# Kernel tuning notes

Hardware: AMD Instinct MI355X
Metric: run time of the kernel (lower is better)

The kernel has to match this reference:

```python
import jax, jax.numpy as jnp
import numpy as np

B, T, H, W, D, NH = 8, 16, 14, 14, 768, 12
HID = int(D * 4.0)
HEAD_DIM = D // NH
EPS = 1e-5


def _ln(x, w, b):
    m = x.mean(-1, keepdims=True)
    v = ((x - m) ** 2).mean(-1, keepdims=True)
    return (x - m) * jax.lax.rsqrt(v + EPS) * w + b


def _attn(x, qkv_w, proj_w, proj_b):
    # x: [Bn, S, D]; qkv_w: [D, 3D] (no bias); proj: [D, D] + bias
    Bn, S, _ = x.shape
    qkv = (x @ qkv_w).reshape(Bn, S, 3, NH, HEAD_DIM).transpose(2, 0, 3, 1, 4)
    q, k, v = qkv[0], qkv[1], qkv[2]
    a = jnp.einsum('bhqd,bhkd->bhqk', q, k) * (HEAD_DIM ** -0.5)
    a = jax.nn.softmax(a, axis=-1)
    o = jnp.einsum('bhqk,bhkd->bhqd', a, v).transpose(0, 2, 1, 3).reshape(Bn, S, D)
    return o @ proj_w + proj_b


def setup_inputs() -> dict:
    key = jax.random.key(0)
    ks = jax.random.split(key, 20)
    N = H * W * T
    s = 0.02
    f32 = jnp.float32
    return {
        'x': jax.random.normal(ks[0], (B, 1 + N, D), f32),
        'tn1_w': jnp.ones((D,), f32), 'tn1_b': jnp.zeros((D,), f32),
        't_qkv_w': jax.random.normal(ks[1], (D, 3 * D), f32) * s,
        't_proj_w': jax.random.normal(ks[2], (D, D), f32) * s,
        't_proj_b': jnp.zeros((D,), f32),
        'tfc_w': jax.random.normal(ks[3], (D, D), f32) * s,
        'tfc_b': jnp.zeros((D,), f32),
        'n1_w': jnp.ones((D,), f32), 'n1_b': jnp.zeros((D,), f32),
        's_qkv_w': jax.random.normal(ks[4], (D, 3 * D), f32) * s,
        's_proj_w': jax.random.normal(ks[5], (D, D), f32) * s,
        's_proj_b': jnp.zeros((D,), f32),
        'n2_w': jnp.ones((D,), f32), 'n2_b': jnp.zeros((D,), f32),
        'fc1_w': jax.random.normal(ks[6], (D, HID), f32) * s,
        'fc1_b': jnp.zeros((HID,), f32),
        'fc2_w': jax.random.normal(ks[7], (HID, D), f32) * s,
        'fc2_b': jnp.zeros((D,), f32),
        'pt_mask': jnp.ones((B, 1 + N), dtype=bool),
        't_frames': T, 'height': H, 'width': W,
    }


def reference(x, tn1_w, tn1_b, t_qkv_w, t_proj_w, t_proj_b, tfc_w, tfc_b,
              n1_w, n1_b, s_qkv_w, s_proj_w, s_proj_b, n2_w, n2_b,
              fc1_w, fc1_b, fc2_w, fc2_b, pt_mask, t_frames, height, width):
    # divided space-time attention; USE_CLS_TOKEN=True, use_pt_visibility=False
    b = x.shape[0]
    t, h, w = t_frames, height, width
    n = h * w * t
    # --- temporal attention over t per (b, h, w) ---
    xt = x[:, 1:, :].reshape(b * h * w, t, D)  # 'b (h w t) m -> (b h w) t m'
    rt = _attn(_ln(xt, tn1_w, tn1_b), t_qkv_w, t_proj_w, t_proj_b)
    rt = rt.reshape(b, n, D) @ tfc_w + tfc_b  # temporal_fc
    xt2 = x[:, 1:, :] + rt
    init_cls = x[:, 0:1, :]  # [b, 1, D]
    # --- spatial attention over (1 + h*w) per (b, t) ---
    cls_tok = jnp.broadcast_to(init_cls, (b, t, D)).reshape(b * t, 1, D)
    xs = xt2.reshape(b, h * w, t, D).transpose(0, 2, 1, 3).reshape(b * t, h * w, D)
    xs = jnp.concatenate([cls_tok, xs], axis=1)  # [(b t), 1+hw, D]
    rs = _attn(_ln(xs, n1_w, n1_b), s_qkv_w, s_proj_w, s_proj_b)
    cls_out = rs[:, 0, :].reshape(b, t, D).mean(axis=1, keepdims=True)
    rs = rs[:, 1:, :].reshape(b, t, h * w, D).transpose(0, 2, 1, 3).reshape(b, n, D)
    x_new = jnp.concatenate([init_cls, xt2], axis=1) + jnp.concatenate([cls_out, rs], axis=1)
    # --- MLP block ---
    y = _ln(x_new, n2_w, n2_b)
    y = jax.nn.gelu(y @ fc1_w + fc1_b, approximate=False) @ fc2_w + fc2_b
    return x_new + y
```

## Files before the change

kernel.cpp:

```cpp
#include <hip/hip_runtime.h>
#include <cstdint>

using u16 = unsigned short;
using u32 = unsigned int;

typedef __bf16 bf16x8 __attribute__((ext_vector_type(8)));
typedef float  floatx4 __attribute__((ext_vector_type(4)));

#define DEV static __device__ __forceinline__

DEV u16 f2bf(float f) {
    u32 u = __float_as_uint(f);
    u += 0x7FFFu + ((u >> 16) & 1u);
    return (u16)(u >> 16);
}
DEV float bf2f(u16 v) { return __uint_as_float(((u32)v) << 16); }

DEV floatx4 mfma32(bf16x8 a, bf16x8 b, floatx4 c) {
    return __builtin_amdgcn_mfma_f32_16x16x32_bf16(a, b, c, 0, 0, 0);
}

DEV floatx4 fzero() { floatx4 z; z[0]=0.f; z[1]=0.f; z[2]=0.f; z[3]=0.f; return z; }

typedef __attribute__((address_space(3))) u32 as3_u32;
typedef __attribute__((address_space(1))) u32 as1_u32;

DEV void async_ld16(const u16* g, u16* l) {
    __builtin_amdgcn_global_load_lds(
        (const as1_u32*)g, (as3_u32*)l, 16, 0, 0);
}

__global__ __launch_bounds__(256) void transpose_w(
    const float* __restrict__ W, u16* __restrict__ Wt, int K, int N)
{
    __shared__ float t[32][33];
    const int tx = threadIdx.x, ty = threadIdx.y;
    const int gx = blockIdx.x * 32;
    const int gy = blockIdx.y * 32;
    #pragma unroll
    for (int i = 0; i < 4; ++i)
        t[ty + i*8][tx] = W[(size_t)(gy + ty + i*8) * N + gx + tx];
    __syncthreads();
    #pragma unroll
    for (int i = 0; i < 4; ++i)
        Wt[(size_t)(gx + ty + i*8) * K + gy + tx] = f2bf(t[tx][ty + i*8]);
}

template<int MODE>
__global__ __launch_bounds__(256) void ln_kernel(
    const float* __restrict__ xp, const u16* __restrict__ xt2,
    const float* __restrict__ w, const float* __restrict__ b,
    u16* __restrict__ out, int nrows)
{
    const int row = blockIdx.x * 4 + (threadIdx.x >> 6);
    if (row >= nrows) return;
    const int lane = threadIdx.x & 63;
    float vals[12];
    if constexpr (MODE == 0) {
        const float* src = xp + (size_t)(row + row/3136 + 1) * 768;
        #pragma unroll
        for (int j = 0; j < 3; ++j) {
            float4 v = reinterpret_cast<const float4*>(src)[j*64 + lane];
            vals[j*4+0]=v.x; vals[j*4+1]=v.y; vals[j*4+2]=v.z; vals[j*4+3]=v.w;
        }
    } else {
        const int bt = row / 197;
        const int p  = row - bt * 197;
        const int b0 = bt >> 4, tt = bt & 15;
        if (p == 0) {
            const float* src = xp + (size_t)b0 * 3137 * 768;
            #pragma unroll
            for (int j = 0; j < 3; ++j) {
                float4 v = reinterpret_cast<const float4*>(src)[j*64 + lane];
                vals[j*4+0]=v.x; vals[j*4+1]=v.y; vals[j*4+2]=v.z; vals[j*4+3]=v.w;
            }
        } else {
            const u16* src = xt2 + (size_t)(b0*3136 + (p-1)*16 + tt) * 768;
            #pragma unroll
            for (int j = 0; j < 3; ++j) {
                uint2 q = reinterpret_cast<const uint2*>(src)[j*64 + lane];
                vals[j*4+0] = bf2f((u16)(q.x & 0xFFFF));
                vals[j*4+1] = bf2f((u16)(q.x >> 16));
                vals[j*4+2] = bf2f((u16)(q.y & 0xFFFF));
                vals[j*4+3] = bf2f((u16)(q.y >> 16));
            }
        }
    }
    float s = 0.f, ss = 0.f;
    #pragma unroll
    for (int e = 0; e < 12; ++e) { s += vals[e]; ss += vals[e]*vals[e]; }
    #pragma unroll
    for (int o = 32; o > 0; o >>= 1) { s += __shfl_xor(s, o); ss += __shfl_xor(ss, o); }
    const float mean = s * (1.f/768.f);
    const float var  = ss * (1.f/768.f) - mean*mean;
    const float rstd = rsqrtf(var + 1e-5f);
    #pragma unroll
    for (int j = 0; j < 3; ++j) {
        const int c4 = (j*64 + lane) * 4;
        union { u16 u[4]; uint2 q; } o;
        #pragma unroll
        for (int e = 0; e < 4; ++e)
            o.u[e] = f2bf((vals[j*4+e] - mean)*rstd*w[c4+e] + b[c4+e]);
        *reinterpret_cast<uint2*>(&out[(size_t)row*768 + c4]) = o.q;
    }
}

__global__ __launch_bounds__(256) void combine_ln2(
    const float* __restrict__ xp, const u16* __restrict__ xt2,
    const u16* __restrict__ rsb, const float* __restrict__ w, const float* __restrict__ b,
    float* __restrict__ xnew, u16* __restrict__ ln2, int nrows)
{
    const int row = blockIdx.x * 4 + (threadIdx.x >> 6);
    if (row >= nrows) return;
    const int lane = threadIdx.x & 63;
    const int b0 = row / 3137;
    const int j  = row - b0 * 3137;
    float vals[12];
    if (j == 0) {
        #pragma unroll
        for (int e = 0; e < 12; ++e) {
            const int c = e*64 + lane;
            float acc = 0.f;
            for (int t = 0; t < 16; ++t)
                acc += bf2f(rsb[(size_t)(b0*16 + t) * 197 * 768 + c]);
            vals[e] = xp[(size_t)row*768 + c] + acc * (1.f/16.f);
        }
    } else {
        const int n_idx = j - 1;
        const int hw = n_idx >> 4, tt = n_idx & 15;
        const u16* a  = xt2 + (size_t)(b0*3136 + n_idx) * 768;
        const u16* r2 = rsb + (size_t)((b0*16 + tt)*197 + 1 + hw) * 768;
        #pragma unroll
        for (int e = 0; e < 12; ++e) {
            const int c = e*64 + lane;
            vals[e] = bf2f(a[c]) + bf2f(r2[c]);
        }
    }
    float s = 0.f, ss = 0.f;
    #pragma unroll
    for (int e = 0; e < 12; ++e) { s += vals[e]; ss += vals[e]*vals[e]; }
    #pragma unroll
    for (int o = 32; o > 0; o >>= 1) { s += __shfl_xor(s, o); ss += __shfl_xor(ss, o); }
    const float mean = s * (1.f/768.f);
    const float var  = ss * (1.f/768.f) - mean*mean;
    const float rstd = rsqrtf(var + 1e-5f);
    #pragma unroll
    for (int e = 0; e < 12; ++e) {
        const int c = e*64 + lane;
        xnew[(size_t)row*768 + c] = vals[e];
        ln2[(size_t)row*768 + c]  = f2bf((vals[e] - mean)*rstd*w[c] + b[c]);
    }
}


#define BARX() do { __builtin_amdgcn_sched_barrier(0); asm volatile("" ::: "memory"); \
    __builtin_amdgcn_s_barrier(); asm volatile("" ::: "memory"); \
    __builtin_amdgcn_sched_barrier(0); } while(0)
#define WAITL() do { asm volatile("s_waitcnt lgkmcnt(0)" ::: "memory"); \
    __builtin_amdgcn_sched_barrier(0); } while(0)
#define WAITV4() do { asm volatile("s_waitcnt vmcnt(4)" ::: "memory"); \
    __builtin_amdgcn_sched_barrier(0); } while(0)
#define WAITV0() do { asm volatile("s_waitcnt vmcnt(0)" ::: "memory"); \
    __builtin_amdgcn_sched_barrier(0); } while(0)

#define RD_A(d, mh) do { \
    _Pragma("unroll") for (int ff = 0; ff < 4; ++ff) { \
      _Pragma("unroll") for (int ks = 0; ks < 2; ++ks) { \
        const int rr = ((mh)*4 + ff)*16 + m15; \
        a[ff*2+ks] = *reinterpret_cast<const bf16x8*>( \
            &sm[(d)*32768 + wm*8192 + rr*64 + ((ks*4 + quad) ^ (m15 & 7))*8]); \
    } } } while(0)

#define RD_B(d, np) do { \
    _Pragma("unroll") for (int nn = 0; nn < 2; ++nn) { \
      _Pragma("unroll") for (int ks = 0; ks < 2; ++ks) { \
        const int rr = (wn & 1)*64 + ((np)*2 + nn)*16 + m15; \
        b[((np)*2 + nn)*2 + ks] = *reinterpret_cast<const bf16x8*>( \
            &sm[(d)*32768 + 16384 + (wn >> 1)*8192 + rr*64 + ((ks*4 + quad) ^ (m15 & 7))*8]); \
    } } } while(0)

#define MQ(F0, NF0) do { \
    _Pragma("unroll") for (int ff = 0; ff < 4; ++ff) { \
      _Pragma("unroll") for (int nn = 0; nn < 2; ++nn) { \
        floatx4 c_ = acc[(F0)+ff][(NF0)+nn]; \
        c_ = mfma32(a[ff*2+0], b[((NF0)+nn)*2+0], c_); \
        c_ = mfma32(a[ff*2+1], b[((NF0)+nn)*2+1], c_); \
        acc[(F0)+ff][(NF0)+nn] = c_; \
    } } } while(0)

#define PRIO1() __builtin_amdgcn_s_setprio(1)
#define PRIO0() __builtin_amdgcn_s_setprio(0)

#define ITER(tt, FULL) do { \
    const int d_ = (tt) & 1; \
     RD_A(d_, 0); RD_B(d_, 0); STAGE((tt)+1, 2); \
    BARX(); WAITL(); PRIO1(); MQ(0,0); PRIO0(); BARX(); \
     RD_B(d_, 1); STAGE((tt)+1, 3); \
    BARX(); WAITL(); PRIO1(); MQ(0,2); PRIO0(); BARX(); \
     RD_A(d_, 1); if (FULL) STAGE((tt)+2, 0); \
    BARX(); WAITL(); PRIO1(); MQ(4,2); PRIO0(); BARX(); \
     if (FULL) STAGE((tt)+2, 1); \
    BARX(); PRIO1(); MQ(4,0); PRIO0(); \
    if (FULL) WAITV4(); else WAITV0(); \
    BARX(); \
     RD_A(d_^1, 0); RD_B(d_^1, 0); if (FULL) STAGE((tt)+2, 2); \
    BARX(); WAITL(); PRIO1(); MQ(0,0); PRIO0(); BARX(); \
     RD_B(d_^1, 1); if (FULL) STAGE((tt)+2, 3); \
    BARX(); WAITL(); PRIO1(); MQ(0,2); PRIO0(); BARX(); \
     RD_A(d_^1, 1); if (FULL) STAGE((tt)+3, 0); \
    BARX(); WAITL(); PRIO1(); MQ(4,2); PRIO0(); BARX(); \
     if (FULL) STAGE((tt)+3, 1); \
    BARX(); PRIO1(); MQ(4,0); PRIO0(); \
    if (FULL) WAITV4(); \
    BARX(); \
} while(0)

template<int RESID, bool BIAS, bool GELU_ACT, bool OUTF, bool OUTB, bool MASKM>
__global__ __launch_bounds__(512, 2) void gemm256(
    const u16* __restrict__ A, const u16* __restrict__ Bt,
    const float* __restrict__ bias, const float* __restrict__ resid,
    float* __restrict__ Cf, u16* __restrict__ Cb,
    int N, int K, int lda, int ldb, int Mvalid)
{
    extern __shared__ u16 sm[];
    const int tid  = threadIdx.x;
    const int w    = tid >> 6;
    const int l    = tid & 63;
    const int m15  = l & 15;
    const int quad = l >> 4;
    const int wm   = w >> 2;
    const int wn   = w & 3;
    const long m0  = (long)blockIdx.y * 256;
    const long n0  = (long)blockIdx.x * 256;

    const int srow   = w*8 + (l >> 3);
    const int schunk = ((l & 7) ^ (l >> 3)) * 8;
    const u16* gA = A  + (size_t)(m0 + srow) * lda + schunk;
    const u16* gB = Bt + (size_t)(n0 + srow) * ldb + schunk;
    const int w512 = w * 512;

    auto STAGE = [&](int tt, int h4) {
        const int dd = tt & 1;
        const int k0 = tt << 6;
        const int h  = h4 & 1;
        if (h4 & 2) {
            const u16* g = gA + (size_t)(h * 128) * lda + k0;
            u16* lp = sm + dd*32768 + h*8192 + w512;
            async_ld16(g, lp);
            async_ld16(g + (size_t)(64 * lda), lp + 4096);
        } else {
            const u16* g = gB + (size_t)(h * 128) * ldb + k0;
            u16* lp = sm + dd*32768 + 16384 + h*8192 + w512;
            async_ld16(g, lp);
            async_ld16(g + (size_t)(64 * ldb), lp + 4096);
        }
    };

    bf16x8 a[8], b[8];
    floatx4 acc[8][4];
    #pragma unroll
    for (int f = 0; f < 8; ++f)
        #pragma unroll
        for (int nf = 0; nf < 4; ++nf) acc[f][nf] = fzero();

    const int NIT = K >> 7;

    STAGE(0, 0); STAGE(0, 1); STAGE(0, 2); STAGE(0, 3);
    STAGE(1, 0); STAGE(1, 1);
    WAITV4(); BARX();

    int t = 0;
    for (int i = 0; i < NIT - 1; ++i, t += 2) { ITER(t, 1); }
    ITER(t, 0);

    float bv[4];
    #pragma unroll
    for (int nf = 0; nf < 4; ++nf)
        bv[nf] = BIAS ? bias[n0 + wn*64 + nf*16 + m15] : 0.f;

    if constexpr (OUTB) {
        u16* cst = sm + w * 8192;
        #pragma unroll
        for (int f = 0; f < 8; ++f) {
            #pragma unroll
            for (int nf = 0; nf < 4; ++nf) {
                #pragma unroll
                for (int r = 0; r < 4; ++r) {
                    const long row = m0 + wm*128 + f*16 + quad*4 + r;
                    float v = acc[f][nf][r] + bv[nf];
                    if constexpr (RESID == 1)
                        v += resid[(size_t)row * N + (n0 + wn*64 + nf*16 + m15)];
                    if constexpr (RESID == 2)
                        v += resid[(size_t)(row + row/3136 + 1) * 768 + (n0 + wn*64 + nf*16 + m15)];
                    if constexpr (GELU_ACT)
                        v = 0.5f * v * (1.f + erff(v * 0.70710678118f));
                    cst[(f*16 + quad*4 + r)*64 + nf*16 + m15] = f2bf(v);
                }
            }
        }
        #pragma unroll
        for (int it = 0; it < 16; ++it) {
            const int lr = it*8 + (l >> 3);
            const long grow = m0 + wm*128 + lr;
            if constexpr (MASKM) { if (grow >= Mvalid) continue; }
            const int cc = (l & 7) * 8;
            *reinterpret_cast<uint4*>(&Cb[(size_t)grow * N + n0 + wn*64 + cc]) =
                *reinterpret_cast<const uint4*>(&cst[lr*64 + cc]);
        }
    } else {
        #pragma unroll
        for (int f = 0; f < 8; ++f) {
            #pragma unroll
            for (int nf = 0; nf < 4; ++nf) {
                const long col = n0 + wn*64 + nf*16 + m15;
                #pragma unroll
                for (int r = 0; r < 4; ++r) {
                    const long row = m0 + wm*128 + f*16 + quad*4 + r;
                    if constexpr (MASKM) { if (row >= Mvalid) continue; }
                    float v = acc[f][nf][r] + bv[nf];
                    if constexpr (RESID == 1) v += resid[(size_t)row * N + col];
                    if constexpr (RESID == 2) v += resid[(size_t)(row + row/3136 + 1) * 768 + col];
                    if constexpr (GELU_ACT)   v = 0.5f * v * (1.f + erff(v * 0.70710678118f));
                    if constexpr (OUTF) Cf[(size_t)row * N + col] = v;
                }
            }
        }
    }
}

template<int S, int NQ, int NIT>
__global__ __launch_bounds__(256) void attn_kernel(
    const u16* __restrict__ qkv, u16* __restrict__ out, int ntask)
{
    __shared__ __attribute__((aligned(16))) u16 P_lds[4][16*32];
    const int wave = threadIdx.x >> 6;
    const int lane = threadIdx.x & 63;
    const int task = blockIdx.x * 4 + wave;
    if (task >= ntask) return;
    const int seq  = task / (12 * NQ);
    const int rem  = task - seq * (12 * NQ);
    const int head = rem / NQ;
    const int qt   = rem - head * NQ;
    const int m15  = lane & 15;
    const int quad = lane >> 4;
    const size_t base = (size_t)seq * S;

    const u16* qp = qkv + (base + qt*16 + m15) * 2304 + head*64 + quad*8;
    const bf16x8 Qf0 = *reinterpret_cast<const bf16x8*>(qp);
    const bf16x8 Qf1 = *reinterpret_cast<const bf16x8*>(qp + 32);

    floatx4 Oacc[4];
    #pragma unroll
    for (int c = 0; c < 4; ++c) Oacc[c] = fzero();
    float mrun = -__builtin_inff();
    float lrun = 0.f;
    u16* P = &P_lds[wave][0];

    for (int it = 0; it < NIT; ++it) {
        const int j0 = it * 32;
        floatx4 st[2];
        #pragma unroll
        for (int h2 = 0; h2 < 2; ++h2) {
            const u16* kp = qkv + (base + j0 + h2*16 + m15) * 2304 + 768 + head*64 + quad*8;
            const bf16x8 K0 = *reinterpret_cast<const bf16x8*>(kp);
            const bf16x8 K1 = *reinterpret_cast<const bf16x8*>(kp + 32);
            floatx4 z = fzero();
            z = mfma32(K0, Qf0, z);
            st[h2] = mfma32(K1, Qf1, z);
        }
        float sc[8];
        #pragma unroll
        for (int h2 = 0; h2 < 2; ++h2)
            #pragma unroll
            for (int r = 0; r < 4; ++r) {
                const int jj = j0 + h2*16 + quad*4 + r;
                sc[h2*4+r] = (jj < S) ? st[h2][r] * 0.125f : -__builtin_inff();
            }
        float tmax = sc[0];
        #pragma unroll
        for (int k = 1; k < 8; ++k) tmax = fmaxf(tmax, sc[k]);
        tmax = fmaxf(tmax, __shfl_xor(tmax, 16));
        tmax = fmaxf(tmax, __shfl_xor(tmax, 32));
        const float mnew = fmaxf(mrun, tmax);
        float p[8], tsum = 0.f;
        #pragma unroll
        for (int k = 0; k < 8; ++k) { p[k] = __expf(sc[k] - mnew); tsum += p[k]; }
        tsum += __shfl_xor(tsum, 16);
        tsum += __shfl_xor(tsum, 32);
        const float alpha = __expf(mrun - mnew);
        lrun = lrun * alpha + tsum;
        mrun = mnew;
        #pragma unroll
        for (int r = 0; r < 4; ++r) {
            const float ar = __shfl(alpha, quad*4 + r);
            #pragma unroll
            for (int c = 0; c < 4; ++c) Oacc[c][r] *= ar;
        }
        #pragma unroll
        for (int h2 = 0; h2 < 2; ++h2)
            #pragma unroll
            for (int r = 0; r < 4; ++r)
                P[m15*32 + h2*16 + quad*4 + r] = f2bf(p[h2*4+r]);
        const bf16x8 Pf = *reinterpret_cast<const bf16x8*>(&P[m15*32 + quad*8]);
        #pragma unroll
        for (int c = 0; c < 4; ++c) {
            union { u16 u[8]; bf16x8 v; } vf;
            #pragma unroll
            for (int jj2 = 0; jj2 < 8; ++jj2)
                vf.u[jj2] = qkv[(base + j0 + quad*8 + jj2) * 2304 + 1536 + head*64 + c*16 + m15];
            Oacc[c] = mfma32(Pf, vf.v, Oacc[c]);
        }
    }
    const float linv_self = 1.f / lrun;
    #pragma unroll
    for (int r = 0; r < 4; ++r) {
        const int prow = qt*16 + quad*4 + r;
        const float linv = __shfl(linv_self, quad*4 + r);
        if (prow < S) {
            u16* op = out + (base + prow) * 768 + head*64 + m15;
            #pragma unroll
            for (int c = 0; c < 4; ++c) op[c*16] = f2bf(Oacc[c][r] * linv);
        }
    }
}

extern "C" void kernel_launch(void* const* d_in, const int* in_sizes, int n_in,
                              void* d_out, int out_size, void* d_ws, size_t ws_size,
                              hipStream_t stream)
{
    (void)in_sizes; (void)n_in; (void)out_size; (void)ws_size;
    const float* x        = (const float*)d_in[0];
    const float* tn1_w    = (const float*)d_in[1];
    const float* tn1_b    = (const float*)d_in[2];
    const float* t_qkv_w  = (const float*)d_in[3];
    const float* t_proj_w = (const float*)d_in[4];
    const float* t_proj_b = (const float*)d_in[5];
    const float* tfc_w    = (const float*)d_in[6];
    const float* tfc_b    = (const float*)d_in[7];
    const float* n1_w     = (const float*)d_in[8];
    const float* n1_b     = (const float*)d_in[9];
    const float* s_qkv_w  = (const float*)d_in[10];
    const float* s_proj_w = (const float*)d_in[11];
    const float* s_proj_b = (const float*)d_in[12];
    const float* n2_w     = (const float*)d_in[13];
    const float* n2_b     = (const float*)d_in[14];
    const float* fc1_w    = (const float*)d_in[15];
    const float* fc1_b    = (const float*)d_in[16];
    const float* fc2_w    = (const float*)d_in[17];
    const float* fc2_b    = (const float*)d_in[18];
    float* out = (float*)d_out;

    char* ws = (char*)d_ws;
    size_t off = 0;
    auto alloc = [&](size_t bytes) -> void* {
        void* p = ws + off;
        off += (bytes + 255) & ~(size_t)255;
        return p;
    };
    u16* wt_tqkv  = (u16*)alloc((size_t)768*2304*2);
    u16* wt_tproj = (u16*)alloc((size_t)768*768*2);
    u16* wt_tfc   = (u16*)alloc((size_t)768*768*2);
    u16* wt_sqkv  = (u16*)alloc((size_t)768*2304*2);
    u16* wt_sproj = (u16*)alloc((size_t)768*768*2);
    u16* wt_fc1   = (u16*)alloc((size_t)768*3072*2);
    u16* wt_fc2   = (u16*)alloc((size_t)3072*768*2);
    u16* slotA = (u16*)alloc((size_t)25280*2304*2);
    u16* slotB = (u16*)alloc((size_t)25216*768*2);
    u16* slotD = (u16*)alloc((size_t)25344*768*2);
    u16* slotE = (u16*)alloc((size_t)25216*768*2);

    dim3 tb(32, 8);
    transpose_w<<<dim3(72, 24), tb, 0, stream>>>(t_qkv_w,  wt_tqkv,  768, 2304);
    transpose_w<<<dim3(24, 24), tb, 0, stream>>>(t_proj_w, wt_tproj, 768, 768);
    transpose_w<<<dim3(24, 24), tb, 0, stream>>>(tfc_w,    wt_tfc,   768, 768);
    transpose_w<<<dim3(72, 24), tb, 0, stream>>>(s_qkv_w,  wt_sqkv,  768, 2304);
    transpose_w<<<dim3(24, 24), tb, 0, stream>>>(s_proj_w, wt_sproj, 768, 768);
    transpose_w<<<dim3(96, 24), tb, 0, stream>>>(fc1_w,    wt_fc1,   768, 3072);
    transpose_w<<<dim3(24, 96), tb, 0, stream>>>(fc2_w,    wt_fc2,   3072, 768);

    const size_t GLDS = 131072;

    u16* lnT  = slotD;
    u16* qkvT = slotA;
    ln_kernel<0><<<25088/4, 256, 0, stream>>>(x, nullptr, tn1_w, tn1_b, lnT, 25088);
    gemm256<0,false,false,false,true,false><<<dim3(9,98), 512, GLDS, stream>>>(
        lnT, wt_tqkv, nullptr, nullptr, nullptr, qkvT, 2304, 768, 768, 768, 0);

    u16* attnT = slotD;
    attn_kernel<16,1,1><<<18816/4, 256, 0, stream>>>(qkvT, attnT, 18816);

    u16* hp = slotE;
    gemm256<0,true,false,false,true,false><<<dim3(3,98), 512, GLDS, stream>>>(
        attnT, wt_tproj, t_proj_b, nullptr, nullptr, hp, 768, 768, 768, 768, 0);

    u16* xt2 = slotB;
    gemm256<2,true,false,false,true,false><<<dim3(3,98), 512, GLDS, stream>>>(
        hp, wt_tfc, tfc_b, x, nullptr, xt2, 768, 768, 768, 768, 0);

    u16* lnS = slotD;
    ln_kernel<1><<<25216/4, 256, 0, stream>>>(x, xt2, n1_w, n1_b, lnS, 25216);

    u16* qkvS = slotA;
    gemm256<0,false,false,false,true,true><<<dim3(9,99), 512, GLDS, stream>>>(
        lnS, wt_sqkv, nullptr, nullptr, nullptr, qkvS, 2304, 768, 768, 768, 25216);

    u16* attnS = slotD;
    attn_kernel<197,13,7><<<19968/4, 256, 0, stream>>>(qkvS, attnS, 19968);

    u16* rsb = slotE;
    gemm256<0,true,false,false,true,true><<<dim3(3,99), 512, GLDS, stream>>>(
        attnS, wt_sproj, s_proj_b, nullptr, nullptr, rsb, 768, 768, 768, 768, 25216);

    float* xnew = out;
    u16* ln2 = slotD;
    combine_ln2<<<25096/4, 256, 0, stream>>>(x, xt2, rsb, n2_w, n2_b, xnew, ln2, 25096);

    u16* h1 = slotA;
    for (int half = 0; half < 2; ++half) {
        const u16* w1h = wt_fc1 + (size_t)half * 1536 * 768;
        const float* b1h = fc1_b + half * 1536;
        gemm256<0,true,true,false,true,true><<<dim3(6,99), 512, GLDS, stream>>>(
            ln2, w1h, b1h, nullptr, nullptr, h1, 1536, 768, 768, 768, 25096);
        const u16* w2h = wt_fc2 + (size_t)half * 1536;
        if (half == 0)
            gemm256<1,true,false,true,false,true><<<dim3(3,99), 512, GLDS, stream>>>(
                h1, w2h, fc2_b, out, out, nullptr, 768, 1536, 1536, 3072, 25096);
        else
            gemm256<1,false,false,true,false,true><<<dim3(3,99), 512, GLDS, stream>>>(
                h1, w2h, nullptr, out, out, nullptr, 768, 1536, 1536, 3072, 25096);
    }
}
```

Measured before the change: 1.297 ms.

## Make GEMMs persistent with contiguous tile ranges and cross-tile prefetch pipeline

Replaces the per-tile 2D-grid GEMM with a persistent kernel launched on 256 blocks. Each block takes a contiguous range of 256x256 output tiles, and a continuous k-step counter lets global-to-LDS prefetch run across tile boundaries. The pipeline is restaged to three in-flight loads with vmcnt(6), and MFMA issue order is changed to interleave k-halves. The bf16 epilogue now writes straight to global, dropping the LDS-staged vectorized 16-byte stores, so bf16 outputs become uncoalesced 2-byte writes. Persistent tiling may also leave load imbalance, because tile counts such as 294 or 297 are not multiples of 256.

Result: slower. 1.488 ms (+14.7%).

```diff
diff --git a/kernel.cpp b/kernel.cpp
--- a/kernel.cpp
+++ b/kernel.cpp
@@ -158,10 +158,12 @@
     __builtin_amdgcn_sched_barrier(0); } while(0)
 #define WAITL() do { asm volatile("s_waitcnt lgkmcnt(0)" ::: "memory"); \
     __builtin_amdgcn_sched_barrier(0); } while(0)
-#define WAITV4() do { asm volatile("s_waitcnt vmcnt(4)" ::: "memory"); \
+#define WAITV6() do { asm volatile("s_waitcnt vmcnt(6)" ::: "memory"); \
     __builtin_amdgcn_sched_barrier(0); } while(0)
 #define WAITV0() do { asm volatile("s_waitcnt vmcnt(0)" ::: "memory"); \
     __builtin_amdgcn_sched_barrier(0); } while(0)
+#define PRIO1() __builtin_amdgcn_s_setprio(1)
+#define PRIO0() __builtin_amdgcn_s_setprio(0)
 
 #define RD_A(d, mh) do { \
     _Pragma("unroll") for (int ff = 0; ff < 4; ++ff) { \
@@ -179,49 +181,32 @@
             &sm[(d)*32768 + 16384 + (wn >> 1)*8192 + rr*64 + ((ks*4 + quad) ^ (m15 & 7))*8]); \
     } } } while(0)
 
-#define MQ(F0, NF0) do { \
-    _Pragma("unroll") for (int ff = 0; ff < 4; ++ff) { \
-      _Pragma("unroll") for (int nn = 0; nn < 2; ++nn) { \
-        floatx4 c_ = acc[(F0)+ff][(NF0)+nn]; \
-        c_ = mfma32(a[ff*2+0], b[((NF0)+nn)*2+0], c_); \
-        c_ = mfma32(a[ff*2+1], b[((NF0)+nn)*2+1], c_); \
-        acc[(F0)+ff][(NF0)+nn] = c_; \
-    } } } while(0)
-
-#define PRIO1() __builtin_amdgcn_s_setprio(1)
-#define PRIO0() __builtin_amdgcn_s_setprio(0)
-
-#define ITER(tt, FULL) do { \
-    const int d_ = (tt) & 1; \
-     RD_A(d_, 0); RD_B(d_, 0); STAGE((tt)+1, 2); \
-    BARX(); WAITL(); PRIO1(); MQ(0,0); PRIO0(); BARX(); \
-     RD_B(d_, 1); STAGE((tt)+1, 3); \
-    BARX(); WAITL(); PRIO1(); MQ(0,2); PRIO0(); BARX(); \
-     RD_A(d_, 1); if (FULL) STAGE((tt)+2, 0); \
-    BARX(); WAITL(); PRIO1(); MQ(4,2); PRIO0(); BARX(); \
-     if (FULL) STAGE((tt)+2, 1); \
-    BARX(); PRIO1(); MQ(4,0); PRIO0(); \
-    if (FULL) WAITV4(); else WAITV0(); \
-    BARX(); \
-     RD_A(d_^1, 0); RD_B(d_^1, 0); if (FULL) STAGE((tt)+2, 2); \
-    BARX(); WAITL(); PRIO1(); MQ(0,0); PRIO0(); BARX(); \
-     RD_B(d_^1, 1); if (FULL) STAGE((tt)+2, 3); \
-    BARX(); WAITL(); PRIO1(); MQ(0,2); PRIO0(); BARX(); \
-     RD_A(d_^1, 1); if (FULL) STAGE((tt)+3, 0); \
-    BARX(); WAITL(); PRIO1(); MQ(4,2); PRIO0(); BARX(); \
-     if (FULL) STAGE((tt)+3, 1); \
-    BARX(); PRIO1(); MQ(4,0); PRIO0(); \
-    if (FULL) WAITV4(); \
-    BARX(); \
-} while(0)
-
-template<int RESID, bool BIAS, bool GELU_ACT, bool OUTF, bool OUTB, bool MASKM>
-__global__ __launch_bounds__(512, 2) void gemm256(
+#define MQk(F0, NF0) do { \
+    _Pragma("unroll") for (int ks = 0; ks < 2; ++ks) { \
+      _Pragma("unroll") for (int ff = 0; ff < 4; ++ff) { \
+        _Pragma("unroll") for (int nn = 0; nn < 2; ++nn) { \
+          acc[(F0)+ff][(NF0)+nn] = \
+            mfma32(a[ff*2+ks], b[((NF0)+nn)*2+ks], acc[(F0)+ff][(NF0)+nn]); \
+    } } } } while(0)
+
+#define PH1(d) do { RD_A(d,0); RD_B(d,0); STG(s+1, 3); \
+    BARX(); WAITL(); PRIO1(); MQk(0,0); PRIO0(); BARX(); } while(0)
+#define PH2(d) do { RD_B(d,1); \
+    BARX(); WAITL(); PRIO1(); MQk(0,2); PRIO0(); BARX(); } while(0)
+#define PH3(d) do { RD_A(d,1); STG(s+2, 0); \
+    BARX(); WAITL(); PRIO1(); MQk(4,2); PRIO0(); BARX(); } while(0)
+#define PH4(d) do { STG(s+2, 1); STG(s+2, 2); \
+    BARX(); PRIO1(); MQk(4,0); PRIO0(); WAITV6(); BARX(); ++s; } while(0)
+
+template<int KSZ, int NTN, int RESID, bool BIAS, bool GELU_ACT, bool OUTF, bool MASKM>
+__global__ __launch_bounds__(512, 2) void gemm_p(
     const u16* __restrict__ A, const u16* __restrict__ Bt,
     const float* __restrict__ bias, const float* __restrict__ resid,
     float* __restrict__ Cf, u16* __restrict__ Cb,
-    int N, int K, int lda, int ldb, int Mvalid)
+    int N, int lda, int ldb, int Mvalid, int ntiles)
 {
+    constexpr int KT = KSZ >> 6;
+    static_assert((KT & 1) == 0, "KT must be even");
     extern __shared__ u16 sm[];
     const int tid  = threadIdx.x;
     const int w    = tid >> 6;
@@ -230,29 +215,40 @@
     const int quad = l >> 4;
     const int wm   = w >> 2;
     const int wn   = w & 3;
-    const long m0  = (long)blockIdx.y * 256;
-    const long n0  = (long)blockIdx.x * 256;
+
+    const int nb   = (int)gridDim.x;
+    const int bid  = (int)blockIdx.x;
+    const int base = ntiles / nb;
+    const int rem  = ntiles - base * nb;
+    const int t0   = bid * base + (bid < rem ? bid : rem);
+    const int len  = base + (bid < rem ? 1 : 0);
+    if (len <= 0) return;
+    const int s_hi = len * KT;
 
     const int srow   = w*8 + (l >> 3);
     const int schunk = ((l & 7) ^ (l >> 3)) * 8;
-    const u16* gA = A  + (size_t)(m0 + srow) * lda + schunk;
-    const u16* gB = Bt + (size_t)(n0 + srow) * ldb + schunk;
-    const int w512 = w * 512;
-
-    auto STAGE = [&](int tt, int h4) {
-        const int dd = tt & 1;
-        const int k0 = tt << 6;
-        const int h  = h4 & 1;
+    const int w512   = w * 512;
+
+    auto STG = [&](int sp, int h4) {
+        const int dd = (sp & 1) * 32768;
+        const int sg = sp < s_hi ? sp : s_hi - 1;
+        const int tau = sg / KT;
+        const int kk  = sg - tau * KT;
+        const int tt  = t0 + tau;
+        const int mt  = tt / NTN;
+        const int nt  = tt - mt * NTN;
+        const int k0  = kk << 6;
+        const int h   = h4 & 1;
         if (h4 & 2) {
-            const u16* g = gA + (size_t)(h * 128) * lda + k0;
-            u16* lp = sm + dd*32768 + h*8192 + w512;
+            const u16* g = A + (size_t)(mt*256 + h*128 + srow) * lda + k0 + schunk;
+            u16* lp = sm + dd + h*8192 + w512;
             async_ld16(g, lp);
-            async_ld16(g + (size_t)(64 * lda), lp + 4096);
+            async_ld16(g + (size_t)64 * lda, lp + 4096);
         } else {
-            const u16* g = gB + (size_t)(h * 128) * ldb + k0;
-            u16* lp = sm + dd*32768 + 16384 + h*8192 + w512;
+            const u16* g = Bt + (size_t)(nt*256 + h*128 + srow) * ldb + k0 + schunk;
+            u16* lp = sm + dd + 16384 + h*8192 + w512;
             async_ld16(g, lp);
-            async_ld16(g + (size_t)(64 * ldb), lp + 4096);
+            async_ld16(g + (size_t)64 * ldb, lp + 4096);
         }
     };
 
@@ -263,69 +259,52 @@
         #pragma unroll
         for (int nf = 0; nf < 4; ++nf) acc[f][nf] = fzero();
 
-    const int NIT = K >> 7;
-
-    STAGE(0, 0); STAGE(0, 1); STAGE(0, 2); STAGE(0, 3);
-    STAGE(1, 0); STAGE(1, 1);
-    WAITV4(); BARX();
-
-    int t = 0;
-    for (int i = 0; i < NIT - 1; ++i, t += 2) { ITER(t, 1); }
-    ITER(t, 0);
-
-    float bv[4];
-    #pragma unroll
-    for (int nf = 0; nf < 4; ++nf)
-        bv[nf] = BIAS ? bias[n0 + wn*64 + nf*16 + m15] : 0.f;
-
-    if constexpr (OUTB) {
-        u16* cst = sm + w * 8192;
-        #pragma unroll
-        for (int f = 0; f < 8; ++f) {
-            #pragma unroll
-            for (int nf = 0; nf < 4; ++nf) {
+    STG(0, 2); STG(0, 0); STG(0, 1); STG(0, 3);
+    STG(1, 0); STG(1, 1); STG(1, 2);
+    WAITV6(); BARX();
+
+    int s = 0;
+    for (int tl = 0; tl < len; ++tl) {
+        #pragma unroll 1
+        for (int k2 = 0; k2 < KT; k2 += 2) {
+            PH1(0); PH2(0); PH3(0); PH4(0);
+            PH1(1); PH2(1); PH3(1); PH4(1);
+        }
+        {
+            const int tt = t0 + tl;
+            const int mt = tt / NTN;
+            const int nt = tt - mt * NTN;
+            const long m0 = (long)mt * 256;
+            const long n0 = (long)nt * 256;
+            float bv[4];
+            #pragma unroll
+            for (int nf = 0; nf < 4; ++nf)
+                bv[nf] = BIAS ? bias[n0 + wn*64 + nf*16 + m15] : 0.f;
+            #pragma unroll
+            for (int f = 0; f < 8; ++f) {
                 #pragma unroll
-                for (int r = 0; r < 4; ++r) {
-                    const long row = m0 + wm*128 + f*16 + quad*4 + r;
-                    float v = acc[f][nf][r] + bv[nf];
-                    if constexpr (RESID == 1)
-                        v += resid[(size_t)row * N + (n0 + wn*64 + nf*16 + m15)];
-                    if constexpr (RESID == 2)
-                        v += resid[(size_t)(row + row/3136 + 1) * 768 + (n0 + wn*64 + nf*16 + m15)];
-                    if constexpr (GELU_ACT)
-                        v = 0.5f * v * (1.f + erff(v * 0.70710678118f));
-                    cst[(f*16 + quad*4 + r)*64 + nf*16 + m15] = f2bf(v);
+                for (int nf = 0; nf < 4; ++nf) {
+                    const long col = n0 + wn*64 + nf*16 + m15;
+                    #pragma unroll
+                    for (int r = 0; r < 4; ++r) {
+                        const long row = m0 + wm*128 + f*16 + quad*4 + r;
+                        if constexpr (MASKM) { if (row >= Mvalid) continue; }
+                        float v = acc[f][nf][r] + bv[nf];
+                        if constexpr (RESID == 1) v += resid[(size_t)row * N + col];
+                        if constexpr (RESID == 2) v += resid[(size_t)(row + row/3136 + 1) * 768 + col];
+                        if constexpr (GELU_ACT)   v = 0.5f * v * (1.f + erff(v * 0.70710678118f));
+                        if constexpr (OUTF) Cf[(size_t)row * N + col] = v;
+                        else                Cb[(size_t)row * N + col] = f2bf(v);
+                    }
                 }
             }
-        }
-        #pragma unroll
-        for (int it = 0; it < 16; ++it) {
-            const int lr = it*8 + (l >> 3);
-            const long grow = m0 + wm*128 + lr;
-            if constexpr (MASKM) { if (grow >= Mvalid) continue; }
-            const int cc = (l & 7) * 8;
-            *reinterpret_cast<uint4*>(&Cb[(size_t)grow * N + n0 + wn*64 + cc]) =
-                *reinterpret_cast<const uint4*>(&cst[lr*64 + cc]);
-        }
-    } else {
-        #pragma unroll
-        for (int f = 0; f < 8; ++f) {
-            #pragma unroll
-            for (int nf = 0; nf < 4; ++nf) {
-                const long col = n0 + wn*64 + nf*16 + m15;
+            #pragma unroll
+            for (int f = 0; f < 8; ++f)
                 #pragma unroll
-                for (int r = 0; r < 4; ++r) {
-                    const long row = m0 + wm*128 + f*16 + quad*4 + r;
-                    if constexpr (MASKM) { if (row >= Mvalid) continue; }
-                    float v = acc[f][nf][r] + bv[nf];
-                    if constexpr (RESID == 1) v += resid[(size_t)row * N + col];
-                    if constexpr (RESID == 2) v += resid[(size_t)(row + row/3136 + 1) * 768 + col];
-                    if constexpr (GELU_ACT)   v = 0.5f * v * (1.f + erff(v * 0.70710678118f));
-                    if constexpr (OUTF) Cf[(size_t)row * N + col] = v;
-                }
-            }
-        }
-    }
+                for (int nf = 0; nf < 4; ++nf) acc[f][nf] = fzero();
+        }
+    }
+    WAITV0();
 }
 
 template<int S, int NQ, int NIT>
@@ -479,37 +458,38 @@
     transpose_w<<<dim3(24, 96), tb, 0, stream>>>(fc2_w,    wt_fc2,   3072, 768);
 
     const size_t GLDS = 131072;
+    const int    GP   = 256;
 
     u16* lnT  = slotD;
     u16* qkvT = slotA;
     ln_kernel<0><<<25088/4, 256, 0, stream>>>(x, nullptr, tn1_w, tn1_b, lnT, 25088);
-    gemm256<0,false,false,false,true,false><<<dim3(9,98), 512, GLDS, stream>>>(
-        lnT, wt_tqkv, nullptr, nullptr, nullptr, qkvT, 2304, 768, 768, 768, 0);
+    gemm_p<768,9,0,false,false,false,false><<<GP, 512, GLDS, stream>>>(
+        lnT, wt_tqkv, nullptr, nullptr, nullptr, qkvT, 2304, 768, 768, 0, 98*9);
 
     u16* attnT = slotD;
     attn_kernel<16,1,1><<<18816/4, 256, 0, stream>>>(qkvT, attnT, 18816);
 
     u16* hp = slotE;
-    gemm256<0,true,false,false,true,false><<<dim3(3,98), 512, GLDS, stream>>>(
-        attnT, wt_tproj, t_proj_b, nullptr, nullptr, hp, 768, 768, 768, 768, 0);
+    gemm_p<768,3,0,true,false,false,false><<<GP, 512, GLDS, stream>>>(
+        attnT, wt_tproj, t_proj_b, nullptr, nullptr, hp, 768, 768, 768, 0, 98*3);
 
     u16* xt2 = slotB;
-    gemm256<2,true,false,false,true,false><<<dim3(3,98), 512, GLDS, stream>>>(
-        hp, wt_tfc, tfc_b, x, nullptr, xt2, 768, 768, 768, 768, 0);
+    gemm_p<768,3,2,true,false,false,false><<<GP, 512, GLDS, stream>>>(
+        hp, wt_tfc, tfc_b, x, nullptr, xt2, 768, 768, 768, 0, 98*3);
 
     u16* lnS = slotD;
     ln_kernel<1><<<25216/4, 256, 0, stream>>>(x, xt2, n1_w, n1_b, lnS, 25216);
 
     u16* qkvS = slotA;
-    gemm256<0,false,false,false,true,true><<<dim3(9,99), 512, GLDS, stream>>>(
-        lnS, wt_sqkv, nullptr, nullptr, nullptr, qkvS, 2304, 768, 768, 768, 25216);
+    gemm_p<768,9,0,false,false,false,true><<<GP, 512, GLDS, stream>>>(
+        lnS, wt_sqkv, nullptr, nullptr, nullptr, qkvS, 2304, 768, 768, 25216, 99*9);
 
     u16* attnS = slotD;
     attn_kernel<197,13,7><<<19968/4, 256, 0, stream>>>(qkvS, attnS, 19968);
 
     u16* rsb = slotE;
-    gemm256<0,true,false,false,true,true><<<dim3(3,99), 512, GLDS, stream>>>(
-        attnS, wt_sproj, s_proj_b, nullptr, nullptr, rsb, 768, 768, 768, 768, 25216);
+    gemm_p<768,3,0,true,false,false,true><<<GP, 512, GLDS, stream>>>(
+        attnS, wt_sproj, s_proj_b, nullptr, nullptr, rsb, 768, 768, 768, 25216, 99*3);
 
     float* xnew = out;
     u16* ln2 = slotD;
@@ -519,14 +499,14 @@
     for (int half = 0; half < 2; ++half) {
         const u16* w1h = wt_fc1 + (size_t)half * 1536 * 768;
         const float* b1h = fc1_b + half * 1536;
-        gemm256<0,true,true,false,true,true><<<dim3(6,99), 512, GLDS, stream>>>(
-            ln2, w1h, b1h, nullptr, nullptr, h1, 1536, 768, 768, 768, 25096);
+        gemm_p<768,6,0,true,true,false,true><<<GP, 512, GLDS, stream>>>(
+            ln2, w1h, b1h, nullptr, nullptr, h1, 1536, 768, 768, 25096, 99*6);
         const u16* w2h = wt_fc2 + (size_t)half * 1536;
         if (half == 0)
-            gemm256<1,true,false,true,false,true><<<dim3(3,99), 512, GLDS, stream>>>(
-                h1, w2h, fc2_b, out, out, nullptr, 768, 1536, 1536, 3072, 25096);
+            gemm_p<1536,3,1,true,false,true,true><<<GP, 512, GLDS, stream>>>(
+                h1, w2h, fc2_b, out, out, nullptr, 768, 1536, 3072, 25096, 99*3);
         else
-            gemm256<1,false,false,true,false,true><<<dim3(3,99), 512, GLDS, stream>>>(
-                h1, w2h, nullptr, out, out, nullptr, 768, 1536, 1536, 3072, 25096);
-    }
-}
+            gemm_p<1536,3,1,false,false,true,true><<<GP, 512, GLDS, stream>>>(
+                h1, w2h, nullptr, out, out, nullptr, 768, 1536, 3072, 25096, 99*3);
+    }
+}
```
